# Kernel optimization log

Measured on AMD Instinct MI355X. Metric: run time of the kernel, lower is better.

Reference implementation:

```python
import jax, jax.numpy as jnp
import numpy as np

SEQ_LEN = 252
FEAT = 21
HID = 128


def setup_inputs() -> dict:
    key = jax.random.key(0)
    ks = jax.random.split(key, 20)
    B = 4096
    values = jax.random.normal(ks[0], (B, SEQ_LEN, FEAT), jnp.float32)
    masks = (jax.random.uniform(ks[1], (B, SEQ_LEN, FEAT)) < 0.8).astype(jnp.float32)
    deltas = jax.random.uniform(ks[2], (B, SEQ_LEN, FEAT), jnp.float32)
    evals = jax.random.normal(ks[3], (B, SEQ_LEN, FEAT), jnp.float32)
    eval_masks = (jax.random.uniform(ks[4], (B, SEQ_LEN, FEAT)) < 0.2).astype(jnp.float32)
    labels = jax.random.normal(ks[5], (B, 1), jnp.float32)
    is_train = (jax.random.uniform(ks[6], (B, 1)) < 0.8).astype(jnp.float32)
    sd = 1.0 / np.sqrt(HID)
    u = lambda k, sh, s: jax.random.uniform(k, sh, jnp.float32, -s, s)
    W_decay = u(ks[7], (HID, FEAT), sd)
    b_decay = u(ks[8], (HID,), sd)
    W_reg = u(ks[9], (FEAT, HID), sd)
    b_reg = u(ks[10], (FEAT,), sd)
    W_ih = u(ks[11], (4 * HID, 2 * FEAT), sd)
    W_hh = u(ks[12], (4 * HID, HID), sd)
    b_ih = u(ks[13], (4 * HID,), sd)
    b_hh = u(ks[14], (4 * HID,), sd)
    W_out = u(ks[15], (1, HID), sd)
    b_out = u(ks[16], (1,), sd)
    return dict(values=values, masks=masks, deltas=deltas, evals=evals,
                eval_masks=eval_masks, labels=labels, is_train=is_train,
                W_decay=W_decay, b_decay=b_decay, W_reg=W_reg, b_reg=b_reg,
                W_ih=W_ih, W_hh=W_hh, b_ih=b_ih, b_hh=b_hh,
                W_out=W_out, b_out=b_out)


def reference(values, masks, deltas, evals, eval_masks, labels, is_train,
              W_decay, b_decay, W_reg, b_reg, W_ih, W_hh, b_ih, b_hh,
              W_out, b_out):
    B = values.shape[0]
    impute_weight, label_weight = 1.0, 1.0
    # time-major [T,B,F] for scan
    xs = (jnp.swapaxes(values, 0, 1), jnp.swapaxes(masks, 0, 1),
          jnp.swapaxes(deltas, 0, 1))
    h0 = jnp.zeros((B, HID), values.dtype)
    c0 = jnp.zeros((B, HID), values.dtype)

    def step(carry, xt):
        h, c, x_loss = carry
        x, m, d = xt
        gamma = jnp.exp(-jax.nn.relu(d @ W_decay.T + b_decay))  # [B,HID]
        h = h * gamma
        x_h = h @ W_reg.T + b_reg                                # [B,FEAT]
        x_c = m * x + (1.0 - m) * x_h
        x_loss = x_loss + jnp.sum(jnp.abs(x - x_h) * m) / (jnp.sum(m) + 1e-5)
        inp = jnp.concatenate([x_c, m], axis=1)                  # [B,2*FEAT]
        gates = inp @ W_ih.T + b_ih + h @ W_hh.T + b_hh          # [B,4*HID]
        i, f, g, o = jnp.split(gates, 4, axis=1)
        c = jax.nn.sigmoid(f) * c + jax.nn.sigmoid(i) * jnp.tanh(g)
        h = jax.nn.sigmoid(o) * jnp.tanh(c)
        return (h, c, x_loss), x_c

    (h, c, x_loss), imp = jax.lax.scan(step, (h0, c0, jnp.float32(0.0)), xs)
    imputations = jnp.swapaxes(imp, 0, 1)                        # [B,T,FEAT]
    y_h = h @ W_out.T + b_out                                    # [B,1]
    y_loss = jnp.sum((y_h - labels) ** 2 * is_train) / (jnp.sum(is_train) + 1e-5)
    loss = x_loss * impute_weight + y_loss * label_weight
    return loss, y_h, imputations
```

## Files before the change

kernel.cpp:

```cpp
#include <hip/hip_runtime.h>
#include <math.h>


#define T_LEN 252
#define FEAT  21
#define HID   128
#define BTOT  4096
#define BT    16
#define NB    (BTOT / BT)
#define NTHR  512
#define LOG2E 1.44269504088896f

#define WS_WHH2   0
#define WS_RDEN   65536
#define WS_XL     65792
#define WS_YNUM   66048
#define WS_YDEN   66304

typedef __attribute__((ext_vector_type(8))) short s16x8;
typedef __attribute__((ext_vector_type(4))) float f32x4;

#define MFMA16(A, B, C) __builtin_amdgcn_mfma_f32_16x16x32_bf16((A), (B), (C), 0, 0, 0)

__device__ __forceinline__ float exp2_f(float x) { return __builtin_amdgcn_exp2f(x); }
__device__ __forceinline__ float rcp_f(float x)  { return __builtin_amdgcn_rcpf(x); }
__device__ __forceinline__ unsigned short to_bf16(float x) {
    unsigned int u = __float_as_uint(x);
    return (unsigned short)((u + 0x7FFFu + ((u >> 16) & 1u)) >> 16);
}
__device__ __forceinline__ unsigned short to_bf16f(float x) {
    return (unsigned short)((__float_as_uint(x) + 0x8000u) >> 16);
}

__global__ __launch_bounds__(1024) void rits_den(
    const float* __restrict__ masks, float* __restrict__ rden)
{
    const int t = blockIdx.x;
    const int tid = threadIdx.x;
    __shared__ float red[1024];
    float acc = 0.0f;
    if (tid < 48 * FEAT) {
        int r0 = tid / FEAT, f = tid - r0 * FEAT;
        for (int r = r0; r < BTOT; r += 48)
            acc += masks[r * (T_LEN * FEAT) + t * FEAT + f];
    }
    red[tid] = acc;
    __syncthreads();
    #pragma unroll
    for (int s = 512; s > 0; s >>= 1) {
        if (tid < s) red[tid] += red[tid + s];
        __syncthreads();
    }
    if (tid == 0) rden[t] = 1.0f / (red[0] + 1e-5f);
}

__global__ __launch_bounds__(256) void rits_fold(
    const float* __restrict__ W_ih, const float* __restrict__ W_hh,
    const float* __restrict__ W_reg, float* __restrict__ whh2)
{
    int idx = blockIdx.x * 256 + threadIdx.x;
    int j4 = idx >> 7, k = idx & (HID - 1);
    float acc = W_hh[j4 * HID + k];
    #pragma unroll
    for (int f = 0; f < FEAT; ++f)
        acc += W_ih[j4 * (2 * FEAT) + f] * W_reg[f * HID + k];
    whh2[idx] = acc;
}

__global__ __launch_bounds__(NTHR, 2) void rits_main(
    const float* __restrict__ values, const float* __restrict__ masks,
    const float* __restrict__ deltas,
    const float* __restrict__ labels, const float* __restrict__ is_train,
    const float* __restrict__ W_decay, const float* __restrict__ b_decay,
    const float* __restrict__ W_reg, const float* __restrict__ b_reg,
    const float* __restrict__ W_ih, const float* __restrict__ W_hh,
    const float* __restrict__ b_ih, const float* __restrict__ b_hh,
    const float* __restrict__ W_out, const float* __restrict__ b_out,
    const float* __restrict__ whh2, const float* __restrict__ rden,
    float* __restrict__ out_yh,
    float* __restrict__ out_imp,
    float* __restrict__ xlpart, float* __restrict__ wsynum, float* __restrict__ wsyden)
{
    const int tid  = threadIdx.x;
    const int blk  = blockIdx.x;
    const int bbase = blk * BT;
    const int l    = tid & 63;
    const int wv   = tid >> 6;
    const int cidx = l & 15;
    const int gidx = l >> 4;
    const int jh   = 16 * wv + cidx;

    __shared__ unsigned short ak_s[2][BT][200];
    __shared__ unsigned short d_s[2][BT][40];
    __shared__ float2 xm_s[3][BT][22];
    __shared__ unsigned short escr_s[8][BT][40];
    __shared__ float hfin_s[BT][HID + 4];
    __shared__ float rden_s[T_LEN];
    __shared__ float red_s[NTHR];

    for (int i = tid; i < 2 * BT * 200; i += NTHR) ((unsigned short*)ak_s)[i] = 0;
    for (int i = tid; i < 2 * BT * 40;  i += NTHR) ((unsigned short*)d_s)[i] = 0;
    for (int i = tid; i < 8 * BT * 40;  i += NTHR) ((unsigned short*)escr_s)[i] = 0;
    if (tid < T_LEN) rden_s[tid] = rden[tid];

    s16x8 bfr_g[4][5], bfr_e[4];
    float bs_r[4];
    #pragma unroll
    for (int g = 0; g < 4; ++g) {
        const float sg = (g == 2) ? (2.0f * LOG2E) : LOG2E;
        const float* rh2 = whh2 + (g * HID + jh) * HID;
        const float* rih = W_ih + (g * HID + jh) * (2 * FEAT);
        #pragma unroll
        for (int s = 0; s < 4; ++s) {
            s16x8 fr;
            #pragma unroll
            for (int j = 0; j < 8; ++j)
                fr[j] = (short)to_bf16(rh2[32 * s + 8 * gidx + j] * sg);
            bfr_g[g][s] = fr;
        }
        {
            s16x8 fr;
            #pragma unroll
            for (int j = 0; j < 8; ++j) {
                int fm = 8 * gidx + j;
                fr[j] = (short)to_bf16(fm < FEAT ? rih[FEAT + fm] * sg : 0.0f);
            }
            bfr_g[g][4] = fr;
        }
        {
            s16x8 fr;
            #pragma unroll
            for (int j = 0; j < 8; ++j) {
                int f = 8 * gidx + j;
                fr[j] = (short)to_bf16(f < FEAT ? rih[f] * sg : 0.0f);
            }
            bfr_e[g] = fr;
        }
        float bb = b_ih[g * HID + jh] + b_hh[g * HID + jh];
        #pragma unroll
        for (int f = 0; f < FEAT; ++f) bb += rih[f] * b_reg[f];
        bs_r[g] = bb * sg;
    }
    s16x8 bfr_d;
    {
        const float* rw = W_decay + jh * FEAT;
        #pragma unroll
        for (int j = 0; j < 8; ++j) {
            int f = 8 * gidx + j;
            bfr_d[j] = (short)to_bf16(f < FEAT ? rw[f] * LOG2E : 0.0f);
        }
    }
    const float bd_r = b_decay[jh] * LOG2E;
    s16x8 bfr_xA[4], bfr_xB[4];
    const bool fBv = (cidx < FEAT - 16);
    #pragma unroll
    for (int s = 0; s < 4; ++s) {
        s16x8 fa, fb;
        #pragma unroll
        for (int j = 0; j < 8; ++j) {
            int k = 32 * s + 8 * gidx + j;
            fa[j] = (short)to_bf16(W_reg[cidx * HID + k]);
            fb[j] = (short)to_bf16(fBv ? W_reg[(16 + cidx) * HID + k] : 0.0f);
        }
        bfr_xA[s] = fa; bfr_xB[s] = fb;
    }
    const float brA = b_reg[cidx];
    const float brB = fBv ? b_reg[16 + cidx] : 0.0f;
    __syncthreads();

    const int st  = tid - 128;
    const bool stg = (st >= 0) && (st < BT * FEAT);
    const int rr = stg ? st / FEAT : 0;
    const int ff = stg ? (st - rr * FEAT) : 0;
    const int rowbase = (bbase + rr) * (T_LEN * FEAT) + ff;
    float nx = 0.f, nm = 0.f, nd = 0.f;
    if (stg) {
        float x0 = values[rowbase], m0 = masks[rowbase];
        xm_s[0][rr][ff] = make_float2(x0, m0);
        ak_s[0][rr][128 + ff] = to_bf16(m0);
        nx = values[rowbase + FEAT];
        nm = masks[rowbase + FEAT];
        nd = deltas[rowbase + FEAT];
    }
    const int ibase = (bbase + 4 * gidx) * (T_LEN * FEAT);
    float c_r[4]   = {0.f, 0.f, 0.f, 0.f};
    float h_r[4]   = {0.f, 0.f, 0.f, 0.f};
    float gam_r[4] = {0.f, 0.f, 0.f, 0.f};
    float xl_acc = 0.0f;
    __syncthreads();

    int bufw = 1;
    int bufr = 0;
    for (int t = 0; t < T_LEN; ++t) {
        const int par = t & 1;

        float lx = 0.f, lm = 0.f, ld = 0.f;
        if (stg) {
            d_s[par ^ 1][rr][ff] = to_bf16f(nd);
            xm_s[bufw][rr][ff] = make_float2(nx, nm);
            int idx = (t + 2 < T_LEN) ? (t + 2) : (T_LEN - 1);
            int o = rowbase + idx * FEAT;
            lx = values[o]; lm = masks[o]; ld = deltas[o];
        }
        #pragma unroll
        for (int v = 0; v < 4; ++v)
            ak_s[par][4 * gidx + v][jh] = to_bf16f(h_r[v] * gam_r[v]);
        __syncthreads();

        s16x8 aF0 = *(const s16x8*)&ak_s[par][cidx][      8 * gidx];
        s16x8 aF1 = *(const s16x8*)&ak_s[par][cidx][ 32 + 8 * gidx];
        s16x8 aF2 = *(const s16x8*)&ak_s[par][cidx][ 64 + 8 * gidx];
        s16x8 aF3 = *(const s16x8*)&ak_s[par][cidx][ 96 + 8 * gidx];
        s16x8 aM  = *(const s16x8*)&ak_s[par][cidx][128 + 8 * gidx];
        s16x8 ad  = *(const s16x8*)&d_s[par ^ 1][cidx][8 * gidx];
        if (stg) ak_s[par ^ 1][rr][128 + ff] = to_bf16f(nm);

        f32x4 xaccA = {brA, brA, brA, brA};
        f32x4 xaccB = {brB, brB, brB, brB};
        xaccA = MFMA16(aF0, bfr_xA[0], xaccA); xaccB = MFMA16(aF0, bfr_xB[0], xaccB);
        xaccA = MFMA16(aF1, bfr_xA[1], xaccA); xaccB = MFMA16(aF1, bfr_xB[1], xaccB);
        xaccA = MFMA16(aF2, bfr_xA[2], xaccA); xaccB = MFMA16(aF2, bfr_xB[2], xaccB);
        xaccA = MFMA16(aF3, bfr_xA[3], xaccA); xaccB = MFMA16(aF3, bfr_xB[3], xaccB);

        const float rd = rden_s[t];
        float eA[4], eB[4];
        #pragma unroll
        for (int v = 0; v < 4; ++v) {
            float2 xm = xm_s[bufr][4 * gidx + v][cidx];
            eA[v] = xm.y * (xm.x - xaccA[v]);
            escr_s[wv][4 * gidx + v][cidx] = to_bf16f(eA[v]);
            if (fBv) {
                float2 xb = xm_s[bufr][4 * gidx + v][16 + cidx];
                eB[v] = xb.y * (xb.x - xaccB[v]);
                escr_s[wv][4 * gidx + v][16 + cidx] = to_bf16f(eB[v]);
            }
        }

        f32x4 acc0 = {bs_r[0], bs_r[0], bs_r[0], bs_r[0]};
        f32x4 acc1 = {bs_r[1], bs_r[1], bs_r[1], bs_r[1]};
        f32x4 acc2 = {bs_r[2], bs_r[2], bs_r[2], bs_r[2]};
        f32x4 acc3 = {bs_r[3], bs_r[3], bs_r[3], bs_r[3]};
        acc0 = MFMA16(aF0, bfr_g[0][0], acc0); acc1 = MFMA16(aF0, bfr_g[1][0], acc1);
        acc2 = MFMA16(aF0, bfr_g[2][0], acc2); acc3 = MFMA16(aF0, bfr_g[3][0], acc3);
        acc0 = MFMA16(aF1, bfr_g[0][1], acc0); acc1 = MFMA16(aF1, bfr_g[1][1], acc1);
        acc2 = MFMA16(aF1, bfr_g[2][1], acc2); acc3 = MFMA16(aF1, bfr_g[3][1], acc3);
        acc0 = MFMA16(aF2, bfr_g[0][2], acc0); acc1 = MFMA16(aF2, bfr_g[1][2], acc1);
        acc2 = MFMA16(aF2, bfr_g[2][2], acc2); acc3 = MFMA16(aF2, bfr_g[3][2], acc3);
        acc0 = MFMA16(aF3, bfr_g[0][3], acc0); acc1 = MFMA16(aF3, bfr_g[1][3], acc1);
        acc2 = MFMA16(aF3, bfr_g[2][3], acc2); acc3 = MFMA16(aF3, bfr_g[3][3], acc3);
        acc0 = MFMA16(aM, bfr_g[0][4], acc0);  acc1 = MFMA16(aM, bfr_g[1][4], acc1);
        acc2 = MFMA16(aM, bfr_g[2][4], acc2);  acc3 = MFMA16(aM, bfr_g[3][4], acc3);
        f32x4 gacc = {bd_r, bd_r, bd_r, bd_r};
        gacc = MFMA16(ad, bfr_d, gacc);

        if (wv == 0) {
            #pragma unroll
            for (int v = 0; v < 4; ++v) {
                out_imp[ibase + v * (T_LEN * FEAT) + t * FEAT + cidx] = xaccA[v] + eA[v];
                xl_acc += fabsf(eA[v]) * rd;
            }
        } else if (wv == 1 && fBv) {
            #pragma unroll
            for (int v = 0; v < 4; ++v) {
                out_imp[ibase + v * (T_LEN * FEAT) + t * FEAT + 16 + cidx] = xaccB[v] + eB[v];
                xl_acc += fabsf(eB[v]) * rd;
            }
        }

        s16x8 eF = *(const s16x8*)&escr_s[wv][cidx][8 * gidx];
        acc0 = MFMA16(eF, bfr_e[0], acc0);
        acc1 = MFMA16(eF, bfr_e[1], acc1);
        acc2 = MFMA16(eF, bfr_e[2], acc2);
        acc3 = MFMA16(eF, bfr_e[3], acc3);

        if (stg) { nx = lx; nm = lm; nd = ld; }

        #pragma unroll
        for (int v = 0; v < 4; ++v) {
            float ig = rcp_f(1.0f + exp2_f(-acc0[v]));
            float fg = rcp_f(1.0f + exp2_f(-acc1[v]));
            float gg = 2.0f * rcp_f(1.0f + exp2_f(-acc2[v])) - 1.0f;
            float og = rcp_f(1.0f + exp2_f(-acc3[v]));
            c_r[v] = fg * c_r[v] + ig * gg;
            float th = 2.0f * rcp_f(1.0f + exp2_f(-2.0f * LOG2E * c_r[v])) - 1.0f;
            h_r[v] = og * th;
            gam_r[v] = exp2_f(-fmaxf(gacc[v], 0.0f));
        }
        int nb = bufw + 1; bufw = (nb > 2) ? 0 : nb;
        int nr = bufr + 1; bufr = (nr > 2) ? 0 : nr;
    }

    #pragma unroll
    for (int v = 0; v < 4; ++v) hfin_s[4 * gidx + v][jh] = h_r[v];
    red_s[tid] = xl_acc;
    __syncthreads();
    #pragma unroll
    for (int s = NTHR / 2; s > 0; s >>= 1) {
        if (tid < s) red_s[tid] += red_s[tid + s];
        __syncthreads();
    }
    if (tid == 0) xlpart[blk] = red_s[0];

    float yerr = 0.0f, ytr = 0.0f;
    if (tid < BT) {
        float acc = b_out[0];
        for (int k = 0; k < HID; ++k) acc += W_out[k] * hfin_s[tid][k];
        out_yh[bbase + tid] = acc;
        float it = is_train[bbase + tid];
        float dv = acc - labels[bbase + tid];
        yerr = dv * dv * it;
        ytr  = it;
    }
    #pragma unroll
    for (int s = 8; s > 0; s >>= 1) {
        yerr += __shfl_down(yerr, s);
        ytr  += __shfl_down(ytr, s);
    }
    if (tid == 0) { wsynum[blk] = yerr; wsyden[blk] = ytr; }
}

__global__ __launch_bounds__(256) void rits_final(
    const float* __restrict__ xlpart,
    const float* __restrict__ wsynum, const float* __restrict__ wsyden,
    float* __restrict__ d_out)
{
    __shared__ float sx[256], sy[256], sz[256];
    int tid = threadIdx.x;
    sx[tid] = xlpart[tid];
    sy[tid] = wsynum[tid];
    sz[tid] = wsyden[tid];
    __syncthreads();
    for (int s = 128; s > 0; s >>= 1) {
        if (tid < s) { sx[tid] += sx[tid + s]; sy[tid] += sy[tid + s]; sz[tid] += sz[tid + s]; }
        __syncthreads();
    }
    if (tid == 0) d_out[0] = sx[0] + sy[0] / (sz[0] + 1e-5f);
}

extern "C" void kernel_launch(void* const* d_in, const int* in_sizes, int n_in,
                              void* d_out, int out_size, void* d_ws, size_t ws_size,
                              hipStream_t stream)
{
    const float* values    = (const float*)d_in[0];
    const float* masks     = (const float*)d_in[1];
    const float* deltas    = (const float*)d_in[2];
    const float* labels    = (const float*)d_in[5];
    const float* is_train  = (const float*)d_in[6];
    const float* W_decay   = (const float*)d_in[7];
    const float* b_decay   = (const float*)d_in[8];
    const float* W_reg     = (const float*)d_in[9];
    const float* b_reg     = (const float*)d_in[10];
    const float* W_ih      = (const float*)d_in[11];
    const float* W_hh      = (const float*)d_in[12];
    const float* b_ih      = (const float*)d_in[13];
    const float* b_hh      = (const float*)d_in[14];
    const float* W_out     = (const float*)d_in[15];
    const float* b_out     = (const float*)d_in[16];

    float* ws     = (float*)d_ws;
    float* whh2   = ws + WS_WHH2;
    float* rden   = ws + WS_RDEN;
    float* xlpart = ws + WS_XL;
    float* wsynum = ws + WS_YNUM;
    float* wsyden = ws + WS_YDEN;

    float* out     = (float*)d_out;
    float* out_yh  = out + 1;
    float* out_imp = out + 1 + BTOT;

    rits_den<<<dim3(T_LEN), dim3(1024), 0, stream>>>(masks, rden);
    rits_fold<<<dim3(256), dim3(256), 0, stream>>>(W_ih, W_hh, W_reg, whh2);

    rits_main<<<dim3(NB), dim3(NTHR), 0, stream>>>(
        values, masks, deltas, labels, is_train,
        W_decay, b_decay, W_reg, b_reg, W_ih, W_hh, b_ih, b_hh, W_out, b_out,
        whh2, rden, out_yh, out_imp, xlpart, wsynum, wsyden);

    rits_final<<<dim3(1), dim3(256), 0, stream>>>(xlpart, wsynum, wsyden, out);
}
```

Baseline: 499.9 us.

## Compute W_reg projection transposed so error fragment stays in registers

Swaps the MFMA operand order for the x_h regression so each lane's accumulator holds features for its own batch row. The error term e can then be packed straight into the A-fragment for the W_ih error MFMA, with no round trip through shared scratch. This removes the escr_s buffer, its stores and its reload, and reorders the W_ih error-column fragments to match the new feature packing. The xm_s row is padded to 33 and the imputation stores now write contiguous features per row, which changes the global write pattern.

```diff
diff --git a/kernel.cpp b/kernel.cpp
--- a/kernel.cpp
+++ b/kernel.cpp
@@ -92,15 +92,14 @@
 
     __shared__ unsigned short ak_s[2][BT][200];
     __shared__ unsigned short d_s[2][BT][40];
-    __shared__ float2 xm_s[3][BT][22];
-    __shared__ unsigned short escr_s[8][BT][40];
+    __shared__ float2 xm_s[3][BT][33];
     __shared__ float hfin_s[BT][HID + 4];
     __shared__ float rden_s[T_LEN];
     __shared__ float red_s[NTHR];
 
     for (int i = tid; i < 2 * BT * 200; i += NTHR) ((unsigned short*)ak_s)[i] = 0;
     for (int i = tid; i < 2 * BT * 40;  i += NTHR) ((unsigned short*)d_s)[i] = 0;
-    for (int i = tid; i < 8 * BT * 40;  i += NTHR) ((unsigned short*)escr_s)[i] = 0;
+    for (int i = tid; i < 3 * BT * 33;  i += NTHR) ((float2*)xm_s)[i] = make_float2(0.f, 0.f);
     if (tid < T_LEN) rden_s[tid] = rden[tid];
 
     s16x8 bfr_g[4][5], bfr_e[4];
@@ -131,7 +130,7 @@
             s16x8 fr;
             #pragma unroll
             for (int j = 0; j < 8; ++j) {
-                int f = 8 * gidx + j;
+                int f = (j < 4) ? (4 * gidx + j) : (16 + 4 * gidx + (j - 4));
                 fr[j] = (short)to_bf16(f < FEAT ? rih[f] * sg : 0.0f);
             }
             bfr_e[g] = fr;
@@ -151,8 +150,7 @@
         }
     }
     const float bd_r = b_decay[jh] * LOG2E;
-    s16x8 bfr_xA[4], bfr_xB[4];
-    const bool fBv = (cidx < FEAT - 16);
+    s16x8 wregT[2][4];
     #pragma unroll
     for (int s = 0; s < 4; ++s) {
         s16x8 fa, fb;
@@ -160,12 +158,17 @@
         for (int j = 0; j < 8; ++j) {
             int k = 32 * s + 8 * gidx + j;
             fa[j] = (short)to_bf16(W_reg[cidx * HID + k]);
-            fb[j] = (short)to_bf16(fBv ? W_reg[(16 + cidx) * HID + k] : 0.0f);
-        }
-        bfr_xA[s] = fa; bfr_xB[s] = fb;
-    }
-    const float brA = b_reg[cidx];
-    const float brB = fBv ? b_reg[16 + cidx] : 0.0f;
+            fb[j] = (short)to_bf16((16 + cidx < FEAT) ? W_reg[(16 + cidx) * HID + k] : 0.0f);
+        }
+        wregT[0][s] = fa; wregT[1][s] = fb;
+    }
+    float brT1[4], brT2[4];
+    #pragma unroll
+    for (int v = 0; v < 4; ++v) {
+        brT1[v] = b_reg[4 * gidx + v];
+        int f2 = 16 + 4 * gidx + v;
+        brT2[v] = (f2 < FEAT) ? b_reg[f2] : 0.0f;
+    }
     __syncthreads();
 
     const int st  = tid - 128;
@@ -182,7 +185,7 @@
         nm = masks[rowbase + FEAT];
         nd = deltas[rowbase + FEAT];
     }
-    const int ibase = (bbase + 4 * gidx) * (T_LEN * FEAT);
+    const int ibase = (bbase + cidx) * (T_LEN * FEAT);
     float c_r[4]   = {0.f, 0.f, 0.f, 0.f};
     float h_r[4]   = {0.f, 0.f, 0.f, 0.f};
     float gam_r[4] = {0.f, 0.f, 0.f, 0.f};
@@ -213,28 +216,20 @@
         s16x8 aF3 = *(const s16x8*)&ak_s[par][cidx][ 96 + 8 * gidx];
         s16x8 aM  = *(const s16x8*)&ak_s[par][cidx][128 + 8 * gidx];
         s16x8 ad  = *(const s16x8*)&d_s[par ^ 1][cidx][8 * gidx];
+        float2 xm1[4], xm2[4];
+        #pragma unroll
+        for (int v = 0; v < 4; ++v) {
+            xm1[v] = xm_s[bufr][cidx][4 * gidx + v];
+            xm2[v] = xm_s[bufr][cidx][16 + 4 * gidx + v];
+        }
         if (stg) ak_s[par ^ 1][rr][128 + ff] = to_bf16f(nm);
 
-        f32x4 xaccA = {brA, brA, brA, brA};
-        f32x4 xaccB = {brB, brB, brB, brB};
-        xaccA = MFMA16(aF0, bfr_xA[0], xaccA); xaccB = MFMA16(aF0, bfr_xB[0], xaccB);
-        xaccA = MFMA16(aF1, bfr_xA[1], xaccA); xaccB = MFMA16(aF1, bfr_xB[1], xaccB);
-        xaccA = MFMA16(aF2, bfr_xA[2], xaccA); xaccB = MFMA16(aF2, bfr_xB[2], xaccB);
-        xaccA = MFMA16(aF3, bfr_xA[3], xaccA); xaccB = MFMA16(aF3, bfr_xB[3], xaccB);
-
-        const float rd = rden_s[t];
-        float eA[4], eB[4];
-        #pragma unroll
-        for (int v = 0; v < 4; ++v) {
-            float2 xm = xm_s[bufr][4 * gidx + v][cidx];
-            eA[v] = xm.y * (xm.x - xaccA[v]);
-            escr_s[wv][4 * gidx + v][cidx] = to_bf16f(eA[v]);
-            if (fBv) {
-                float2 xb = xm_s[bufr][4 * gidx + v][16 + cidx];
-                eB[v] = xb.y * (xb.x - xaccB[v]);
-                escr_s[wv][4 * gidx + v][16 + cidx] = to_bf16f(eB[v]);
-            }
-        }
+        f32x4 xaccT1 = {brT1[0], brT1[1], brT1[2], brT1[3]};
+        f32x4 xaccT2 = {brT2[0], brT2[1], brT2[2], brT2[3]};
+        xaccT1 = MFMA16(wregT[0][0], aF0, xaccT1); xaccT2 = MFMA16(wregT[1][0], aF0, xaccT2);
+        xaccT1 = MFMA16(wregT[0][1], aF1, xaccT1); xaccT2 = MFMA16(wregT[1][1], aF1, xaccT2);
+        xaccT1 = MFMA16(wregT[0][2], aF2, xaccT1); xaccT2 = MFMA16(wregT[1][2], aF2, xaccT2);
+        xaccT1 = MFMA16(wregT[0][3], aF3, xaccT1); xaccT2 = MFMA16(wregT[1][3], aF3, xaccT2);
 
         f32x4 acc0 = {bs_r[0], bs_r[0], bs_r[0], bs_r[0]};
         f32x4 acc1 = {bs_r[1], bs_r[1], bs_r[1], bs_r[1]};
@@ -253,25 +248,37 @@
         f32x4 gacc = {bd_r, bd_r, bd_r, bd_r};
         gacc = MFMA16(ad, bfr_d, gacc);
 
-        if (wv == 0) {
-            #pragma unroll
-            for (int v = 0; v < 4; ++v) {
-                out_imp[ibase + v * (T_LEN * FEAT) + t * FEAT + cidx] = xaccA[v] + eA[v];
-                xl_acc += fabsf(eA[v]) * rd;
-            }
-        } else if (wv == 1 && fBv) {
-            #pragma unroll
-            for (int v = 0; v < 4; ++v) {
-                out_imp[ibase + v * (T_LEN * FEAT) + t * FEAT + 16 + cidx] = xaccB[v] + eB[v];
-                xl_acc += fabsf(eB[v]) * rd;
-            }
-        }
-
-        s16x8 eF = *(const s16x8*)&escr_s[wv][cidx][8 * gidx];
+        float e1[4], e2[4];
+        s16x8 eF;
+        #pragma unroll
+        for (int v = 0; v < 4; ++v) {
+            e1[v] = xm1[v].y * (xm1[v].x - xaccT1[v]);
+            e2[v] = xm2[v].y * (xm2[v].x - xaccT2[v]);
+            eF[v]     = (short)to_bf16f(e1[v]);
+            eF[4 + v] = (short)to_bf16f(e2[v]);
+        }
         acc0 = MFMA16(eF, bfr_e[0], acc0);
         acc1 = MFMA16(eF, bfr_e[1], acc1);
         acc2 = MFMA16(eF, bfr_e[2], acc2);
         acc3 = MFMA16(eF, bfr_e[3], acc3);
+
+        const float rd = rden_s[t];
+        if (wv == 0) {
+            #pragma unroll
+            for (int v = 0; v < 4; ++v) {
+                out_imp[ibase + t * FEAT + 4 * gidx + v] = xaccT1[v] + e1[v];
+                xl_acc += fabsf(e1[v]) * rd;
+            }
+        } else if (wv == 1) {
+            #pragma unroll
+            for (int v = 0; v < 4; ++v) {
+                int f2 = 16 + 4 * gidx + v;
+                if (f2 < FEAT) {
+                    out_imp[ibase + t * FEAT + f2] = xaccT2[v] + e2[v];
+                    xl_acc += fabsf(e2[v]) * rd;
+                }
+            }
+        }
 
         if (stg) { nx = lx; nm = lm; nd = ld; }
 
```

Measured after the change: 452.8 us. -9.4%, faster.
